# Optimization experiments

Measured on AMD Instinct MI355X. Metric: run time of the kernel, lower is better.

Reference implementation:

```python
import jax, jax.numpy as jnp
import numpy as np

NEG = jnp.float32(-1e30)  # max-plus identity (finite to keep grads clean)


def setup_inputs() -> dict:
    key = jax.random.key(0)
    k1, k2 = jax.random.split(key)
    B, Cin, H, W = 8, 64, 64, 64
    Cout, kH, kW = 64, 3, 3
    x = jax.random.normal(k1, (B, Cin, H, W), dtype=jnp.float32)
    weight = jax.random.normal(k2, (Cout, Cin, kH, kW), dtype=jnp.float32)
    return {"x": x, "weight": weight, "kernel_size": 3, "padding": 1}


def reference(x, weight, kernel_size, padding):
    # Max-plus correlation (tropical conv), stride 1:
    #   out[b,co,y,x] = max_{ci,i,j} ( x_pad[b,ci,y+i,x+j] + weight[co,ci,i,j] )
    kH = kW = int(kernel_size)
    padH = padW = int(padding)
    B, Cin, H, W = x.shape
    Cout = weight.shape[0]
    xp = jnp.pad(x, ((0, 0), (0, 0), (padH, padH), (padW, padW)),
                 constant_values=NEG)  # -inf-like padding: identity of max
    Ho = H + 2 * padH - kH + 1
    Wo = W + 2 * padW - kW + 1
    out = jnp.full((B, Cout, Ho, Wo), NEG, dtype=x.dtype)
    for i in range(kH):          # small fixed kernel loop (kH*kW taps)
        for j in range(kW):
            win = xp[:, :, i:i + Ho, j:j + Wo]            # [B,Ci,Ho,Wo]
            cand = win[:, None] + weight[None, :, :, i, j, None, None]
            out = jnp.maximum(out, cand.max(axis=2))      # reduce over Ci
    return out
```

## Files before the change

### kernel.cpp

```cpp
#include <hip/hip_runtime.h>

#define NEGV -1e30f

constexpr int Bn = 8, Ci = 64, Hn = 64, Wn = 64, Co = 64;

constexpr int G  = 4;
constexpr int CW = Wn / G;

__global__ __launch_bounds__(256)
void wtrans_kernel(const float* __restrict__ wt, float* __restrict__ wT) {
    int idx = blockIdx.x * 256 + threadIdx.x;
    if (idx < Ci * 9 * Co) {
        int co = idx & 63;
        int k  = (idx >> 6) % 9;
        int ci = idx / (9 * Co);
        wT[idx] = wt[((size_t)co * Ci + ci) * 9 + k];
    }
}

template<int EDGE>
__device__ __forceinline__ void load6(float* xv, const float* __restrict__ p) {
    if (EDGE == 1) {
        xv[0] = NEGV;
#pragma unroll
        for (int c = 1; c < 6; c++) xv[c] = p[c - 1];
    } else if (EDGE == 2) {
#pragma unroll
        for (int c = 0; c < 5; c++) xv[c] = p[c];
        xv[5] = NEGV;
    } else {
#pragma unroll
        for (int c = 0; c < 6; c++) xv[c] = p[c];
    }
}

template<int EDGE>
__device__ __forceinline__ void run_wave(const float* __restrict__ x,
                                         const float* __restrict__ wT,
                                         float* __restrict__ out,
                                         int b, int h, int w0, int lane) {
    const bool hasUp = (h > 0);
    const bool hasDn = (h < Hn - 1);
    const int  cb    = (EDGE == 1) ? 0 : (w0 - 1);

    const float* px = x + (((size_t)b * Ci) * Hn + h) * Wn + cb;
    const float* pw = wT + lane;

    float a[G];
#pragma unroll
    for (int p = 0; p < G; p++) a[p] = NEGV;

    for (int ci = 0; ci < Ci; ci++, px += Hn * Wn, pw += 9 * Co) {
        float xu[6], xc[6], xd[6];
        load6<EDGE>(xc, px);
        if (hasUp) load6<EDGE>(xu, px - Wn);
        else {
#pragma unroll
            for (int c = 0; c < 6; c++) xu[c] = NEGV;
        }
        if (hasDn) load6<EDGE>(xd, px + Wn);
        else {
#pragma unroll
            for (int c = 0; c < 6; c++) xd[c] = NEGV;
        }

        float wv[9];
#pragma unroll
        for (int k = 0; k < 9; k++) wv[k] = pw[k * Co];

#pragma unroll
        for (int p = 0; p < G; p++) {
            float t0 = xu[p] + wv[0], t1 = xu[p + 1] + wv[1], t2 = xu[p + 2] + wv[2];
            float t3 = xc[p] + wv[3], t4 = xc[p + 1] + wv[4], t5 = xc[p + 2] + wv[5];
            float t6 = xd[p] + wv[6], t7 = xd[p + 1] + wv[7], t8 = xd[p + 2] + wv[8];
            float v = a[p];
            v = fmaxf(v, fmaxf(t0, t1));
            v = fmaxf(v, fmaxf(t2, t3));
            v = fmaxf(v, fmaxf(t4, t5));
            v = fmaxf(v, fmaxf(t6, t7));
            v = fmaxf(v, t8);
            a[p] = v;
        }
    }

    float4 st = make_float4(a[0], a[1], a[2], a[3]);
    *reinterpret_cast<float4*>(out + (((size_t)b * Co + lane) * Hn + h) * Wn + w0) = st;
}

__global__ __launch_bounds__(256, 8)
void maxconv_main(const float* __restrict__ x, const float* __restrict__ wT,
                  float* __restrict__ out) {
    const int lane = threadIdx.x & 63;
    const int wid  = threadIdx.x >> 6;
    const int cw   = __builtin_amdgcn_readfirstlane(blockIdx.x * 4 + wid);
    const int w0   = cw * G;
    const int h    = blockIdx.y;
    const int b    = blockIdx.z;

    if (cw == 0)           run_wave<1>(x, wT, out, b, h, w0, lane);
    else if (cw == CW - 1) run_wave<2>(x, wT, out, b, h, w0, lane);
    else                   run_wave<0>(x, wT, out, b, h, w0, lane);
}

extern "C" void kernel_launch(void* const* d_in, const int* in_sizes, int n_in,
                              void* d_out, int out_size, void* d_ws, size_t ws_size,
                              hipStream_t stream) {
    const float* x  = (const float*)d_in[0];
    const float* wt = (const float*)d_in[1];
    float* out = (float*)d_out;
    float* wT  = (float*)d_ws;

    wtrans_kernel<<<(Ci * 9 * Co + 255) / 256, 256, 0, stream>>>(wt, wT);

    dim3 grid(CW / 4, Hn, Bn);
    maxconv_main<<<grid, 256, 0, stream>>>(x, wT, out);
}
```

Before: 122.8 us.

## Software-pipeline weight loads across channels and use v_max3 reductions

Restructures the channel loop into a two-stage software pipeline: the weights for the next input channel are loaded one step ahead into alternating register sets, and the loop is unrolled by two and marked unroll 1. The max reduction now uses inline v_max3_f32 assembly, cutting the max instruction count per output. This aims to hide global load latency and reduce VALU work, at the cost of more registers under the existing launch bounds of 8 blocks. Inline asm may also limit compiler scheduling.

```diff
diff --git a/kernel.cpp b/kernel.cpp
--- a/kernel.cpp
+++ b/kernel.cpp
@@ -18,6 +18,12 @@
     }
 }
 
+__device__ __forceinline__ float vmax3(float a, float b, float c) {
+    float d;
+    asm("v_max3_f32 %0, %1, %2, %3" : "=v"(d) : "v"(a), "v"(b), "v"(c));
+    return d;
+}
+
 template<int EDGE>
 __device__ __forceinline__ void load6(float* xv, const float* __restrict__ p) {
     if (EDGE == 1) {
@@ -34,6 +40,44 @@
     }
 }
 
+struct Win { float u[6], c[6], d[6]; };
+
+template<int EDGE>
+__device__ __forceinline__ void loadwin(Win& w, const float* __restrict__ px,
+                                        bool hasUp, bool hasDn) {
+    load6<EDGE>(w.c, px);
+    if (hasUp) load6<EDGE>(w.u, px - Wn);
+    else {
+#pragma unroll
+        for (int c = 0; c < 6; c++) w.u[c] = NEGV;
+    }
+    if (hasDn) load6<EDGE>(w.d, px + Wn);
+    else {
+#pragma unroll
+        for (int c = 0; c < 6; c++) w.d[c] = NEGV;
+    }
+}
+
+__device__ __forceinline__ void loadw(float* wv, const float* __restrict__ wrow,
+                                      int lane) {
+#pragma unroll
+    for (int k = 0; k < 9; k++) wv[k] = wrow[k * Co + lane];
+}
+
+__device__ __forceinline__ void compute(float* a, const Win& w, const float* wv) {
+#pragma unroll
+    for (int p = 0; p < G; p++) {
+        float t0 = w.u[p] + wv[0], t1 = w.u[p + 1] + wv[1], t2 = w.u[p + 2] + wv[2];
+        float t3 = w.c[p] + wv[3], t4 = w.c[p + 1] + wv[4], t5 = w.c[p + 2] + wv[5];
+        float t6 = w.d[p] + wv[6], t7 = w.d[p + 1] + wv[7], t8 = w.d[p + 2] + wv[8];
+        float m0 = vmax3(t0, t1, t2);
+        float m1 = vmax3(t3, t4, t5);
+        float m2 = vmax3(t6, t7, t8);
+        a[p] = vmax3(a[p], m0, m1);
+        a[p] = fmaxf(a[p], m2);
+    }
+}
+
 template<int EDGE>
 __device__ __forceinline__ void run_wave(const float* __restrict__ x,
                                          const float* __restrict__ wT,
@@ -43,45 +87,32 @@
     const bool hasDn = (h < Hn - 1);
     const int  cb    = (EDGE == 1) ? 0 : (w0 - 1);
 
-    const float* px = x + (((size_t)b * Ci) * Hn + h) * Wn + cb;
-    const float* pw = wT + lane;
+    const float* px   = x + (((size_t)b * Ci) * Hn + h) * Wn + cb;
+    const float* wrow = wT;
 
     float a[G];
 #pragma unroll
     for (int p = 0; p < G; p++) a[p] = NEGV;
 
-    for (int ci = 0; ci < Ci; ci++, px += Hn * Wn, pw += 9 * Co) {
-        float xu[6], xc[6], xd[6];
-        load6<EDGE>(xc, px);
-        if (hasUp) load6<EDGE>(xu, px - Wn);
-        else {
-#pragma unroll
-            for (int c = 0; c < 6; c++) xu[c] = NEGV;
-        }
-        if (hasDn) load6<EDGE>(xd, px + Wn);
-        else {
-#pragma unroll
-            for (int c = 0; c < 6; c++) xd[c] = NEGV;
-        }
+    Win wA, wB;
+    float vA[9], vB[9];
 
-        float wv[9];
-#pragma unroll
-        for (int k = 0; k < 9; k++) wv[k] = pw[k * Co];
+    loadw(vA, wrow, lane);  wrow += 9 * Co;
 
-#pragma unroll
-        for (int p = 0; p < G; p++) {
-            float t0 = xu[p] + wv[0], t1 = xu[p + 1] + wv[1], t2 = xu[p + 2] + wv[2];
-            float t3 = xc[p] + wv[3], t4 = xc[p + 1] + wv[4], t5 = xc[p + 2] + wv[5];
-            float t6 = xd[p] + wv[6], t7 = xd[p + 1] + wv[7], t8 = xd[p + 2] + wv[8];
-            float v = a[p];
-            v = fmaxf(v, fmaxf(t0, t1));
-            v = fmaxf(v, fmaxf(t2, t3));
-            v = fmaxf(v, fmaxf(t4, t5));
-            v = fmaxf(v, fmaxf(t6, t7));
-            v = fmaxf(v, t8);
-            a[p] = v;
-        }
+#pragma unroll 1
+    for (int ci = 0; ci < Ci - 2; ci += 2) {
+        loadw(vB, wrow, lane);  wrow += 9 * Co;
+        loadwin<EDGE>(wA, px, hasUp, hasDn);  px += Hn * Wn;
+        compute(a, wA, vA);
+        loadw(vA, wrow, lane);  wrow += 9 * Co;
+        loadwin<EDGE>(wB, px, hasUp, hasDn);  px += Hn * Wn;
+        compute(a, wB, vB);
     }
+    loadw(vB, wrow, lane);
+    loadwin<EDGE>(wA, px, hasUp, hasDn);  px += Hn * Wn;
+    compute(a, wA, vA);
+    loadwin<EDGE>(wB, px, hasUp, hasDn);
+    compute(a, wB, vB);
 
     float4 st = make_float4(a[0], a[1], a[2], a[3]);
     *reinterpret_cast<float4*>(out + (((size_t)b * Co + lane) * Hn + h) * Wn + w0) = st;
```

Result: no change. 122.0 us (-0.6%).

## Stage input halo tile in LDS and widen per-thread output to 8 columns

Applied to the files above, without the earlier changes.

Each block now cooperatively loads a 3-row by 34-column halo tile for all 64 input channels into shared memory, padding with the max-plus identity, before computing. Each wave then produces 8 output columns per thread instead of 4, reading its window from LDS with vector loads and reducing with v_max3 instructions. A swizzled 1D grid mapping and a 2-channel unrolled loop replace the per-edge template branches. This cuts redundant global loads of x and halves the weight loads per output, at the cost of a syncthreads, about 30KB of LDS per block, and lower declared occupancy.

```diff
diff --git a/kernel.cpp b/kernel.cpp
--- a/kernel.cpp
+++ b/kernel.cpp
@@ -3,103 +3,122 @@
 #define NEGV -1e30f
 
 constexpr int Bn = 8, Ci = 64, Hn = 64, Wn = 64, Co = 64;
-
-constexpr int G  = 4;
-constexpr int CW = Wn / G;
+constexpr int WT_ELEMS = Ci * 9 * Co;
 
 __global__ __launch_bounds__(256)
 void wtrans_kernel(const float* __restrict__ wt, float* __restrict__ wT) {
     int idx = blockIdx.x * 256 + threadIdx.x;
-    if (idx < Ci * 9 * Co) {
+    if (idx < WT_ELEMS) {
         int co = idx & 63;
         int k  = (idx >> 6) % 9;
-        int ci = idx / (9 * Co);
+        int ci = idx / 576;
         wT[idx] = wt[((size_t)co * Ci + ci) * 9 + k];
     }
 }
 
-template<int EDGE>
-__device__ __forceinline__ void load6(float* xv, const float* __restrict__ p) {
-    if (EDGE == 1) {
-        xv[0] = NEGV;
+__device__ __forceinline__ float vmax3(float a, float b, float c) {
+    float d;
+    asm("v_max3_f32 %0, %1, %2, %3" : "=v"(d) : "v"(a), "v"(b), "v"(c));
+    return d;
+}
+
+__device__ __forceinline__ void read10(float* o, const float* __restrict__ p) {
+    float4 a = *reinterpret_cast<const float4*>(p);
+    float4 b = *reinterpret_cast<const float4*>(p + 4);
+    float2 c = *reinterpret_cast<const float2*>(p + 8);
+    o[0] = a.x; o[1] = a.y; o[2] = a.z; o[3] = a.w;
+    o[4] = b.x; o[5] = b.y; o[6] = b.z; o[7] = b.w;
+    o[8] = c.x; o[9] = c.y;
+}
+
+__device__ __forceinline__ void compute8(float* acc, const float* xu,
+                                         const float* xc, const float* xd,
+                                         const float* wv) {
 #pragma unroll
-        for (int c = 1; c < 6; c++) xv[c] = p[c - 1];
-    } else if (EDGE == 2) {
-#pragma unroll
-        for (int c = 0; c < 5; c++) xv[c] = p[c];
-        xv[5] = NEGV;
-    } else {
-#pragma unroll
-        for (int c = 0; c < 6; c++) xv[c] = p[c];
+    for (int j = 0; j < 8; j++) {
+        float t0 = xu[j] + wv[0], t1 = xu[j + 1] + wv[1], t2 = xu[j + 2] + wv[2];
+        float t3 = xc[j] + wv[3], t4 = xc[j + 1] + wv[4], t5 = xc[j + 2] + wv[5];
+        float t6 = xd[j] + wv[6], t7 = xd[j + 1] + wv[7], t8 = xd[j + 2] + wv[8];
+        float m0 = vmax3(t0, t1, t2);
+        float m1 = vmax3(t3, t4, t5);
+        float m2 = vmax3(t6, t7, t8);
+        acc[j] = vmax3(acc[j], m0, m1);
+        acc[j] = fmaxf(acc[j], m2);
     }
 }
 
-template<int EDGE>
-__device__ __forceinline__ void run_wave(const float* __restrict__ x,
-                                         const float* __restrict__ wT,
-                                         float* __restrict__ out,
-                                         int b, int h, int w0, int lane) {
-    const bool hasUp = (h > 0);
-    const bool hasDn = (h < Hn - 1);
-    const int  cb    = (EDGE == 1) ? 0 : (w0 - 1);
+__global__ __launch_bounds__(256, 4)
+void maxconv_main(const float* __restrict__ x, const float* __restrict__ wT,
+                  float* __restrict__ out) {
+    __shared__ __align__(16) float xs[Ci * 120];
 
-    const float* px = x + (((size_t)b * Ci) * Hn + h) * Wn + cb;
-    const float* pw = wT + lane;
+    const int tid  = threadIdx.x;
+    const int lane = tid & 63;
+    const int wvid = tid >> 6;
 
-    float a[G];
+    const int lg   = ((blockIdx.x & 7) << 7) | (blockIdx.x >> 3);
+    const int b    = lg >> 7;
+    const int rem  = lg & 127;
+    const int h    = rem >> 1;
+    const int half = rem & 1;
+    const int w0h  = half << 5;
+
+    {
+        const int st     = (tid < 128) ? tid : tid - 128;
+        const int cibase = (tid < 128) ? 0 : 32;
+        if (st < 102) {
+            const int r    = st / 34;
+            const int s    = st - r * 34;
+            const int grow = h - 1 + r;
+            const int gcol = w0h - 1 + s;
+            const bool valid = (grow >= 0) && (grow < Hn) && (gcol >= 0) && (gcol < Wn);
+            const int cg   = valid ? grow : 0;
+            const int cc   = valid ? gcol : 0;
+            const float* gp = x + (((size_t)b * Ci + cibase) * Hn + cg) * Wn + cc;
+            const int dst  = r * 40 + s;
+#pragma unroll 1
+            for (int c8 = 0; c8 < 32; c8 += 8) {
+                float v[8];
 #pragma unroll
-    for (int p = 0; p < G; p++) a[p] = NEGV;
+                for (int i = 0; i < 8; i++)
+                    v[i] = valid ? gp[(size_t)(c8 + i) * Hn * Wn] : NEGV;
+#pragma unroll
+                for (int i = 0; i < 8; i++)
+                    xs[(cibase + c8 + i) * 120 + dst] = v[i];
+            }
+        }
+    }
+    __syncthreads();
 
-    for (int ci = 0; ci < Ci; ci++, px += Hn * Wn, pw += 9 * Co) {
-        float xu[6], xc[6], xd[6];
-        load6<EDGE>(xc, px);
-        if (hasUp) load6<EDGE>(xu, px - Wn);
-        else {
+    const int woff = wvid * 8;
+
+    float acc[8];
 #pragma unroll
-            for (int c = 0; c < 6; c++) xu[c] = NEGV;
-        }
-        if (hasDn) load6<EDGE>(xd, px + Wn);
-        else {
-#pragma unroll
-            for (int c = 0; c < 6; c++) xd[c] = NEGV;
-        }
+    for (int j = 0; j < 8; j++) acc[j] = NEGV;
 
+#pragma unroll 1
+    for (int ci = 0; ci < Ci; ci += 2) {
+        const float* wrow = wT + ci * 576;
         float wv[9];
 #pragma unroll
-        for (int k = 0; k < 9; k++) wv[k] = pw[k * Co];
+        for (int k = 0; k < 9; k++) wv[k] = wrow[k * 64 + lane];
+        float xu[10], xc[10], xd[10];
+        const float* base0 = xs + ci * 120 + woff;
+        read10(xu, base0); read10(xc, base0 + 40); read10(xd, base0 + 80);
+        compute8(acc, xu, xc, xd, wv);
 
+        const float* wrow2 = wrow + 576;
+        float wv2[9];
 #pragma unroll
-        for (int p = 0; p < G; p++) {
-            float t0 = xu[p] + wv[0], t1 = xu[p + 1] + wv[1], t2 = xu[p + 2] + wv[2];
-            float t3 = xc[p] + wv[3], t4 = xc[p + 1] + wv[4], t5 = xc[p + 2] + wv[5];
-            float t6 = xd[p] + wv[6], t7 = xd[p + 1] + wv[7], t8 = xd[p + 2] + wv[8];
-            float v = a[p];
-            v = fmaxf(v, fmaxf(t0, t1));
-            v = fmaxf(v, fmaxf(t2, t3));
-            v = fmaxf(v, fmaxf(t4, t5));
-            v = fmaxf(v, fmaxf(t6, t7));
-            v = fmaxf(v, t8);
-            a[p] = v;
-        }
+        for (int k = 0; k < 9; k++) wv2[k] = wrow2[k * 64 + lane];
+        const float* base1 = base0 + 120;
+        read10(xu, base1); read10(xc, base1 + 40); read10(xd, base1 + 80);
+        compute8(acc, xu, xc, xd, wv2);
     }
 
-    float4 st = make_float4(a[0], a[1], a[2], a[3]);
-    *reinterpret_cast<float4*>(out + (((size_t)b * Co + lane) * Hn + h) * Wn + w0) = st;
-}
-
-__global__ __launch_bounds__(256, 8)
-void maxconv_main(const float* __restrict__ x, const float* __restrict__ wT,
-                  float* __restrict__ out) {
-    const int lane = threadIdx.x & 63;
-    const int wid  = threadIdx.x >> 6;
-    const int cw   = __builtin_amdgcn_readfirstlane(blockIdx.x * 4 + wid);
-    const int w0   = cw * G;
-    const int h    = blockIdx.y;
-    const int b    = blockIdx.z;
-
-    if (cw == 0)           run_wave<1>(x, wT, out, b, h, w0, lane);
-    else if (cw == CW - 1) run_wave<2>(x, wT, out, b, h, w0, lane);
-    else                   run_wave<0>(x, wT, out, b, h, w0, lane);
+    float* po = out + (((size_t)b * Co + lane) * Hn + h) * Wn + w0h + woff;
+    *reinterpret_cast<float4*>(po)     = make_float4(acc[0], acc[1], acc[2], acc[3]);
+    *reinterpret_cast<float4*>(po + 4) = make_float4(acc[4], acc[5], acc[6], acc[7]);
 }
 
 extern "C" void kernel_launch(void* const* d_in, const int* in_sizes, int n_in,
@@ -110,8 +129,7 @@
     float* out = (float*)d_out;
     float* wT  = (float*)d_ws;
 
-    wtrans_kernel<<<(Ci * 9 * Co + 255) / 256, 256, 0, stream>>>(wt, wT);
+    wtrans_kernel<<<(WT_ELEMS + 255) / 256, 256, 0, stream>>>(wt, wT);
 
-    dim3 grid(CW / 4, Hn, Bn);
-    maxconv_main<<<grid, 256, 0, stream>>>(x, wT, out);
+    maxconv_main<<<1024, 256, 0, stream>>>(x, wT, out);
 }
```

Measured after the change: 114.8 us. -6.5%, faster.
